# Performance work log

Measured on AMD Instinct MI355X. Metric: run time of the kernel, lower is better.

Reference implementation:

```python
import jax, jax.numpy as jnp
import numpy as np
from itertools import combinations

N = 128
D = 512
EPSILON = 32.0
VR_DIM = 2
SHARPNESS = 10.0


def _pairwise_dist(W):
    # [N, N] Euclidean distance matrix via GEMM
    sq = jnp.sum(W * W, axis=1)
    d2 = sq[:, None] + sq[None, :] - 2.0 * (W @ W.T)
    return jnp.sqrt(jnp.maximum(d2, 0.0))


def setup_inputs() -> dict:
    key = jax.random.key(0)
    W = jax.random.normal(key, (N, D), dtype=jnp.float32)
    return {"W": W}


def reference(W) -> jnp.ndarray:
    n = W.shape[0]
    dist = _pairwise_dist(W)  # [N, N]

    # 0-simplices: identity masks
    m0 = jnp.eye(n, dtype=W.dtype)

    # 1-simplices: soft sigmoid value at both endpoints of every pair
    iu, ju = np.triu_indices(n, k=1)  # static index arrays, P = C(N,2)
    P = iu.shape[0]
    d_pair = dist[iu, ju]
    # 1/(1+exp(s*(d-eps))) == sigmoid(s*(eps-d))
    val = jax.nn.sigmoid(SHARPNESS * (EPSILON - d_pair))
    rp = np.arange(P)
    m1 = jnp.zeros((P, n), dtype=W.dtype).at[rp, iu].set(val).at[rp, ju].set(val)

    parts = [m0, m1]

    if VR_DIM >= 2:
        # 2-simplices: hard indicator masks on all triples (zero row if not formed)
        tri = np.array(list(combinations(range(n), 3)), dtype=np.int32)  # [T, 3]
        ti, tj, tk = tri[:, 0], tri[:, 1], tri[:, 2]
        T = tri.shape[0]
        cond = (
            (dist[ti, tj] <= EPSILON)
            & (dist[tj, tk] <= EPSILON)
            & (dist[ti, tk] <= EPSILON)
        ).astype(W.dtype)
        rt = np.arange(T)
        m2 = (
            jnp.zeros((T, n), dtype=W.dtype)
            .at[rt, ti].set(cond)
            .at[rt, tj].set(cond)
            .at[rt, tk].set(cond)
        )
        parts.append(m2)

    return jnp.concatenate(parts, axis=0)
```

## Files before the change

### kernel.cpp

```cpp
#include <hip/hip_runtime.h>
#include <math.h>

#define NPTS      128
#define DIM       512
#define NPAIR     8128
#define NTRI      341376
#define ROW_PAIR0 128
#define ROW_TRI0  8256
#define NROWS     349632
#define FILL_BLOCKS 1366

__global__ __launch_bounds__(64) void vr_dist_kernel(
    const float* __restrict__ W,
    float* __restrict__ sigval,
    unsigned long long* __restrict__ adj) {
    __shared__ float wi[DIM];
    const int i    = blockIdx.x >> 1;
    const int half = blockIdx.x & 1;
    const int lane = threadIdx.x;
    const int j    = (half << 6) + lane;
    for (int c = lane; c < DIM; c += 64) wi[c] = W[i * DIM + c];
    __syncthreads();

    const float4* wj4 = (const float4*)(W + (size_t)j * DIM);
    const float4* wi4 = (const float4*)wi;
    double a0 = 0.0, a1 = 0.0, a2 = 0.0, a3 = 0.0;
    #pragma unroll 4
    for (int c = 0; c < DIM / 4; ++c) {
        float4 a = wi4[c];
        float4 b = wj4[c];
        double d0 = (double)a.x - (double)b.x;
        double d1 = (double)a.y - (double)b.y;
        double d2 = (double)a.z - (double)b.z;
        double d3 = (double)a.w - (double)b.w;
        a0 = fma(d0, d0, a0);
        a1 = fma(d1, d1, a1);
        a2 = fma(d2, d2, a2);
        a3 = fma(d3, d3, a3);
    }
    double dist = sqrt((a0 + a1) + (a2 + a3));

    unsigned long long m = __ballot(dist <= 32.0);
    if (lane == 0) adj[i * 2 + half] = m;

    if (j > i) {
        int p = 127 * i - ((i * (i - 1)) >> 1) + (j - i - 1);
        float x = 10.0f * (32.0f - (float)dist);
        sigval[p] = 1.0f / (1.0f + expf(-x));
    }
}

__global__ __launch_bounds__(256) void vr_fill_kernel(
    const float* __restrict__ sigval,
    const unsigned long long* __restrict__ adj,
    float4* __restrict__ out) {
    __shared__ unsigned long long sadj[256];
    __shared__ unsigned int smask[256][4];
    __shared__ float sval[256];

    const int tid = threadIdx.x;
    sadj[tid] = adj[tid];
    __syncthreads();

    const int row0 = blockIdx.x * 256;
    const int row  = row0 + tid;

    int a = 255, b = 255, c = 255;
    float val = 0.0f;
    if (row < ROW_PAIR0) {
        a = row; val = 1.0f;
    } else if (row < ROW_TRI0) {
        int p = row - ROW_PAIR0;
        int lo = 0, hi = 127;
        #pragma unroll
        for (int it = 0; it < 7; ++it) {
            int m = (lo + hi + 1) >> 1;
            int C = 127 * m - ((m * (m - 1)) >> 1);
            if (C <= p) lo = m; else hi = m - 1;
        }
        a = lo;
        b = a + 1 + (p - (127 * a - ((a * (a - 1)) >> 1)));
        val = sigval[p];
    } else if (row < NROWS) {
        int t = row - ROW_TRI0;
        int lo = 0, hi = 125;
        #pragma unroll
        for (int it = 0; it < 7; ++it) {
            int m = (lo + hi + 1) >> 1;
            int rem = NPTS - m;
            int T = NTRI - rem * (rem - 1) * (rem - 2) / 6;
            if (T <= t) lo = m; else hi = m - 1;
        }
        a = lo;
        int rema = NPTS - a;
        int r = t - (NTRI - rema * (rema - 1) * (rema - 2) / 6);
        lo = a + 1; hi = 126;
        #pragma unroll
        for (int it = 0; it < 7; ++it) {
            int m = (lo + hi + 1) >> 1;
            int C2 = ((m - a - 1) * (254 - a - m)) >> 1;
            if (C2 <= r) lo = m; else hi = m - 1;
        }
        b = lo;
        c = b + 1 + (r - (((b - a - 1) * (254 - a - b)) >> 1));

        unsigned long long bab = sadj[(a << 1) + (b >> 6)] >> (b & 63);
        unsigned long long bbc = sadj[(b << 1) + (c >> 6)] >> (c & 63);
        unsigned long long bac = sadj[(a << 1) + (c >> 6)] >> (c & 63);
        val = (float)(bab & bbc & bac & 1ull);
    }
    #pragma unroll
    for (int w = 0; w < 4; ++w) {
        unsigned int mw = 0;
        mw |= ((a >> 5) == w) ? (1u << (a & 31)) : 0u;
        mw |= ((b >> 5) == w) ? (1u << (b & 31)) : 0u;
        mw |= ((c >> 5) == w) ? (1u << (c & 31)) : 0u;
        smask[tid][w] = mw;
    }
    sval[tid] = val;
    __syncthreads();

    const int col4 = tid & 31;
    const int rsub = tid >> 5;
    const int widx = col4 >> 3;
    const int sh   = (col4 & 7) << 2;

    float4* p = out + (size_t)(row0 + rsub) * 32 + col4;

    #pragma unroll 4
    for (int k = 0; k < 32; ++k) {
        int rl = (k << 3) + rsub;
        unsigned int nib = smask[rl][widx] >> sh;
        float vv = sval[rl];

        float4 v;
        v.x = (nib & 1u) ? vv : 0.0f;
        v.y = (nib & 2u) ? vv : 0.0f;
        v.z = (nib & 4u) ? vv : 0.0f;
        v.w = (nib & 8u) ? vv : 0.0f;

        if (row0 + rl < NROWS) p[(size_t)k * 256] = v;
    }
}

extern "C" void kernel_launch(void* const* d_in, const int* in_sizes, int n_in,
                              void* d_out, int out_size, void* d_ws, size_t ws_size,
                              hipStream_t stream) {
    const float* W = (const float*)d_in[0];
    float* out = (float*)d_out;

    unsigned long long* adj = (unsigned long long*)d_ws;
    float* sigval = (float*)((char*)d_ws + 2048);

    vr_dist_kernel<<<256, 64, 0, stream>>>(W, sigval, adj);
    vr_fill_kernel<<<FILL_BLOCKS, 256, 0, stream>>>(sigval, adj, (float4*)out);
}
```

Before: 192.0 us.

## Zero-fill output tiles with streaming stores, then scatter nonzero entries

```diff
diff --git a/kernel.cpp b/kernel.cpp
--- a/kernel.cpp
+++ b/kernel.cpp
@@ -8,7 +8,8 @@
 #define ROW_PAIR0 128
 #define ROW_TRI0  8256
 #define NROWS     349632
-#define FILL_BLOCKS 1366
+#define TILE      192
+#define FILL_BLOCKS 1821
 
 __global__ __launch_bounds__(64) void vr_dist_kernel(
     const float* __restrict__ W,
@@ -53,93 +54,83 @@
 __global__ __launch_bounds__(256) void vr_fill_kernel(
     const float* __restrict__ sigval,
     const unsigned long long* __restrict__ adj,
-    float4* __restrict__ out) {
-    __shared__ unsigned long long sadj[256];
-    __shared__ unsigned int smask[256][4];
-    __shared__ float sval[256];
+    float* __restrict__ out) {
+    const int tid  = threadIdx.x;
+    const int row0 = blockIdx.x * TILE;
+    const int row  = row0 + tid;
 
-    const int tid = threadIdx.x;
-    sadj[tid] = adj[tid];
+    int kind = 0;
+    int a = 0, b = 0, c = 0;
+    unsigned long long wab = 0, wbc = 0, wac = 0;
+    float sv = 0.0f;
+
+    if (tid < TILE) {
+        if (row < ROW_PAIR0) {
+            kind = 1; a = row;
+        } else if (row < ROW_TRI0) {
+            kind = 2;
+            int p = row - ROW_PAIR0;
+            int lo = 0, hi = 127;
+            #pragma unroll
+            for (int it = 0; it < 7; ++it) {
+                int m = (lo + hi + 1) >> 1;
+                int C = 127 * m - ((m * (m - 1)) >> 1);
+                if (C <= p) lo = m; else hi = m - 1;
+            }
+            a = lo;
+            b = a + 1 + (p - (127 * a - ((a * (a - 1)) >> 1)));
+            sv = sigval[p];
+        } else {
+            kind = 3;
+            int t = row - ROW_TRI0;
+            int lo = 0, hi = 125;
+            #pragma unroll
+            for (int it = 0; it < 7; ++it) {
+                int m = (lo + hi + 1) >> 1;
+                int rem = NPTS - m;
+                int T = NTRI - rem * (rem - 1) * (rem - 2) / 6;
+                if (T <= t) lo = m; else hi = m - 1;
+            }
+            a = lo;
+            int rema = NPTS - a;
+            int r = t - (NTRI - rema * (rema - 1) * (rema - 2) / 6);
+            lo = a + 1; hi = 126;
+            #pragma unroll
+            for (int it = 0; it < 7; ++it) {
+                int m = (lo + hi + 1) >> 1;
+                int C2 = ((m - a - 1) * (254 - a - m)) >> 1;
+                if (C2 <= r) lo = m; else hi = m - 1;
+            }
+            b = lo;
+            c = b + 1 + (r - (((b - a - 1) * (254 - a - b)) >> 1));
+            wab = adj[(a << 1) + (b >> 6)];
+            wbc = adj[(b << 1) + (c >> 6)];
+            wac = adj[(a << 1) + (c >> 6)];
+        }
+    }
+
+    const float4 z = make_float4(0.0f, 0.0f, 0.0f, 0.0f);
+    float4* slab = (float4*)out + (size_t)blockIdx.x * (TILE * 32);
+    #pragma unroll
+    for (int k = 0; k < (TILE * 32) / 256; ++k)
+        slab[k * 256 + tid] = z;
+
     __syncthreads();
 
-    const int row0 = blockIdx.x * 256;
-    const int row  = row0 + tid;
-
-    int a = 255, b = 255, c = 255;
-    float val = 0.0f;
-    if (row < ROW_PAIR0) {
-        a = row; val = 1.0f;
-    } else if (row < ROW_TRI0) {
-        int p = row - ROW_PAIR0;
-        int lo = 0, hi = 127;
-        #pragma unroll
-        for (int it = 0; it < 7; ++it) {
-            int m = (lo + hi + 1) >> 1;
-            int C = 127 * m - ((m * (m - 1)) >> 1);
-            if (C <= p) lo = m; else hi = m - 1;
+    float* rp = out + (size_t)row * NPTS;
+    if (kind == 1) {
+        rp[a] = 1.0f;
+    } else if (kind == 2) {
+        rp[a] = sv;
+        rp[b] = sv;
+    } else if (kind == 3) {
+        unsigned long long ok = (wab >> (b & 63)) & (wbc >> (c & 63)) &
+                                (wac >> (c & 63)) & 1ull;
+        if (ok) {
+            rp[a] = 1.0f;
+            rp[b] = 1.0f;
+            rp[c] = 1.0f;
         }
-        a = lo;
-        b = a + 1 + (p - (127 * a - ((a * (a - 1)) >> 1)));
-        val = sigval[p];
-    } else if (row < NROWS) {
-        int t = row - ROW_TRI0;
-        int lo = 0, hi = 125;
-        #pragma unroll
-        for (int it = 0; it < 7; ++it) {
-            int m = (lo + hi + 1) >> 1;
-            int rem = NPTS - m;
-            int T = NTRI - rem * (rem - 1) * (rem - 2) / 6;
-            if (T <= t) lo = m; else hi = m - 1;
-        }
-        a = lo;
-        int rema = NPTS - a;
-        int r = t - (NTRI - rema * (rema - 1) * (rema - 2) / 6);
-        lo = a + 1; hi = 126;
-        #pragma unroll
-        for (int it = 0; it < 7; ++it) {
-            int m = (lo + hi + 1) >> 1;
-            int C2 = ((m - a - 1) * (254 - a - m)) >> 1;
-            if (C2 <= r) lo = m; else hi = m - 1;
-        }
-        b = lo;
-        c = b + 1 + (r - (((b - a - 1) * (254 - a - b)) >> 1));
-
-        unsigned long long bab = sadj[(a << 1) + (b >> 6)] >> (b & 63);
-        unsigned long long bbc = sadj[(b << 1) + (c >> 6)] >> (c & 63);
-        unsigned long long bac = sadj[(a << 1) + (c >> 6)] >> (c & 63);
-        val = (float)(bab & bbc & bac & 1ull);
-    }
-    #pragma unroll
-    for (int w = 0; w < 4; ++w) {
-        unsigned int mw = 0;
-        mw |= ((a >> 5) == w) ? (1u << (a & 31)) : 0u;
-        mw |= ((b >> 5) == w) ? (1u << (b & 31)) : 0u;
-        mw |= ((c >> 5) == w) ? (1u << (c & 31)) : 0u;
-        smask[tid][w] = mw;
-    }
-    sval[tid] = val;
-    __syncthreads();
-
-    const int col4 = tid & 31;
-    const int rsub = tid >> 5;
-    const int widx = col4 >> 3;
-    const int sh   = (col4 & 7) << 2;
-
-    float4* p = out + (size_t)(row0 + rsub) * 32 + col4;
-
-    #pragma unroll 4
-    for (int k = 0; k < 32; ++k) {
-        int rl = (k << 3) + rsub;
-        unsigned int nib = smask[rl][widx] >> sh;
-        float vv = sval[rl];
-
-        float4 v;
-        v.x = (nib & 1u) ? vv : 0.0f;
-        v.y = (nib & 2u) ? vv : 0.0f;
-        v.z = (nib & 4u) ? vv : 0.0f;
-        v.w = (nib & 8u) ? vv : 0.0f;
-
-        if (row0 + rl < NROWS) p[(size_t)k * 256] = v;
     }
 }
 
@@ -153,5 +144,5 @@
     float* sigval = (float*)((char*)d_ws + 2048);
 
     vr_dist_kernel<<<256, 64, 0, stream>>>(W, sigval, adj);
-    vr_fill_kernel<<<FILL_BLOCKS, 256, 0, stream>>>(sigval, adj, (float4*)out);
+    vr_fill_kernel<<<FILL_BLOCKS, 256, 0, stream>>>(sigval, adj, out);
 }
```

Result: no change. 190.5 us (-0.8%).
